# Performance work log

Hardware: AMD Instinct MI355X
Metric: run time of the kernel (lower is better)

The kernel has to match this reference:

```python
import jax, jax.numpy as jnp
import numpy as np

C = 16       # celltypes
N = 20000    # nodes per PPI graph
D = 192      # in_channels == out_channels*heads (residual constraint)
H = 3        # node_heads
CO = 64      # out_channels per head
E = 320000   # edges per PPI graph
T = 32       # tissue nodes
K = 8        # neighbors per tissue
M = C + T    # metagraph nodes
R = 4        # metagraph relations
EM = 256     # edges per metagraph relation
S = 128      # sem_att_channels
TU = 100     # tissue_update iterations


def setup_inputs():
    key = jax.random.key(0)
    k = jax.random.split(key, 16)
    g = lambda kk, shp, sc: jax.random.normal(kk, shp, jnp.float32) * sc
    return {
        "ppi_x": g(k[0], (C, N, D), 1.0),
        "metagraph_x": g(k[1], (M, D), 1.0),
        "ppi_lin": g(k[2], (C, D, H * CO), 0.07),
        "ppi_att_src": g(k[3], (C, H, CO), 0.1),
        "ppi_att_dst": g(k[4], (C, H, CO), 0.1),
        "ppi_bias": jnp.zeros((C, H * CO), jnp.float32),
        "meta_lin": g(k[5], (R, H * CO, H * CO), 0.07),
        "meta_att_src": g(k[6], (R, H, CO), 0.1),
        "meta_att_dst": g(k[7], (R, H, CO), 0.1),
        "meta_bias": jnp.zeros((R, H * CO), jnp.float32),
        "W_sem": g(k[8], (H * CO, S), 0.08),
        "b_sem": jnp.zeros((S,), jnp.float32),
        "q_sem": g(k[9], (S,), 0.1),
        "ppi_edges": jax.random.randint(k[10], (C, 2, E), 0, N, dtype=jnp.int32),
        "meta_edges": jax.random.randint(k[11], (R, 2, EM), 0, M, dtype=jnp.int32),
        "tissue_nb": jax.random.randint(k[12], (T, K), 0, M, dtype=jnp.int32),
    }


def gat(x, lin, att_s, att_d, bias, edge, n):
    """PyG-style GATConv, concat heads. x:[n,Din], edge:[2,E] (src,dst)."""
    h = (x @ lin).reshape(n, H, CO)
    a_s = (h * att_s).sum(-1)   # [n,H]
    a_d = (h * att_d).sum(-1)
    src, dst = edge[0], edge[1]
    e = jax.nn.leaky_relu(a_s[src] + a_d[dst], negative_slope=0.2)  # [E,H]
    emax = jax.lax.stop_gradient(jax.ops.segment_max(e, dst, num_segments=n))
    emax = jnp.where(jnp.isfinite(emax), emax, 0.0)
    ex = jnp.exp(e - emax[dst])
    denom = jax.ops.segment_sum(ex, dst, num_segments=n)          # [n,H]
    out = jax.ops.segment_sum(ex[:, :, None] * h[src], dst, num_segments=n)
    out = out / jnp.where(denom > 0.0, denom, 1.0)[:, :, None]
    return out.reshape(n, H * CO) + bias


def sem_attention(out, W, b, q):
    """Semantic attention over relations. out:[M,R,Dh]."""
    w = jnp.tanh(jnp.einsum('mrd,ds->mrs', out, W) + b)
    beta = jax.nn.softmax(jnp.einsum('mrs,s->mr', w, q), axis=1)
    return jnp.einsum('mrd,mr->md', out, beta)


def forward(ppi_x, metagraph_x, ppi_lin, ppi_att_src, ppi_att_dst, ppi_bias,
            meta_lin, meta_att_src, meta_att_dst, meta_bias,
            W_sem, b_sem, q_sem, ppi_edges, meta_edges, tissue_nb):
    mx = metagraph_x
    # residual GAT per celltype, mean-pooled into the metagraph celltype row
    for c in range(C):
        att = ppi_x[c] + gat(ppi_x[c], ppi_lin[c], ppi_att_src[c], ppi_att_dst[c],
                             ppi_bias[c], ppi_edges[c], N)
        mx = mx.at[c].add(att.mean(0))
    # sequential (Gauss-Seidel) tissue-neighbor mean diffusion, TU sweeps
    def step(m, t):
        return m.at[C + t].set(m[tissue_nb[t]].mean(0)), None
    def sweep(m, _):
        m, _ = jax.lax.scan(step, m, jnp.arange(T))
        return m, None
    mx, _ = jax.lax.scan(sweep, mx, None, length=TU)
    # multi-relation metagraph GAT + semantic attention fusion
    outs = jnp.stack([gat(mx, meta_lin[r], meta_att_src[r], meta_att_dst[r],
                          meta_bias[r], meta_edges[r], M) for r in range(R)], axis=1)
    outs = jax.nn.relu(outs)  # torch applies relu after stacking
    return sem_attention(outs, W_sem, b_sem, q_sem)


def reference(ppi_x, metagraph_x, ppi_lin, ppi_att_src, ppi_att_dst, ppi_bias,
              meta_lin, meta_att_src, meta_att_dst, meta_bias,
              W_sem, b_sem, q_sem, ppi_edges, meta_edges, tissue_nb):
    return forward(ppi_x, metagraph_x, ppi_lin, ppi_att_src, ppi_att_dst, ppi_bias,
                   meta_lin, meta_att_src, meta_att_dst, meta_bias,
                   W_sem, b_sem, q_sem, ppi_edges, meta_edges, tissue_nb)
```

## Files before the change

kernel.cpp:

```cpp
#include <hip/hip_runtime.h>

#define CT 16
#define NN 20000
#define EE 320000
#define MM 48
#define RR 4
#define EMM 256
#define NRANGE 64
#define NPR 313
#define CAP 5632
#define MAGIC 13721941ULL

#define OFF_MEANX 0
#define OFF_P     3072
#define OFF_CNTD  12288
#define OFF_CNTS  13312
#define ZERO_FLOATS 14336
#define OFF_COMB  14336
#define OFF_AS    2574336
#define OFF_AD    3854336
#define OFF_U     5134336
#define OFF_V     5143552
#define OFF_MX    5152768
#define OFF_HH    5161984
#define OFF_OUTS  5198848
#define OFF_BIND  5235712
#define OFF_BINS  11002880
#define OFF_W     16770048
#define OFF_MX2   16772352

__device__ inline unsigned bucket_of(int d) {
    return (unsigned)(((unsigned long long)(unsigned)d * MAGIC) >> 32);
}

__global__ __launch_bounds__(192) void k_prep(const float* __restrict__ lin,
        const float* __restrict__ as_g, const float* __restrict__ ad_g,
        float* __restrict__ U, float* __restrict__ V, float* __restrict__ zws) {
    int c = blockIdx.x, d = threadIdx.x;
    int gt = c * 192 + d;
    for (int o = gt; o < ZERO_FLOATS; o += 16 * 192) zws[o] = 0.f;
    const float* L  = lin + ((size_t)c * 192 + d) * 192;
    const float* As = as_g + c * 192;
    const float* Ad = ad_g + c * 192;
#pragma unroll
    for (int h = 0; h < 3; ++h) {
        float u = 0.f, v = 0.f;
        for (int j = 0; j < 64; ++j) {
            float lv = L[h * 64 + j];
            u += lv * As[h * 64 + j];
            v += lv * Ad[h * 64 + j];
        }
        U[c * 576 + h * 192 + d] = u;
        V[c * 576 + h * 192 + d] = v;
    }
}

__global__ __launch_bounds__(256) void k_front(const int* __restrict__ edges,
        int* __restrict__ cntD, int* __restrict__ cntS,
        int* __restrict__ binD, int* __restrict__ binS,
        const float* __restrict__ x, const float* __restrict__ U,
        const float* __restrict__ V, float* __restrict__ a_s,
        float* __restrict__ a_d, float* __restrict__ meanx) {
    __shared__ __align__(16) float smem[3456];
    int tid = threadIdx.x;
    if (blockIdx.x < 1024) {
        int wg = blockIdx.x;
        int ct = (wg & 7) * 2 + ((wg >> 3) & 1);
        int part = wg >> 4;
        int wave = tid >> 6;
        int* histD = (int*)smem;
        int* histS = histD + 256;
        int* curD  = histS + 256;
        int* curS  = curD + 64;
        if (tid < NRANGE) {
            histD[0 * 64 + tid] = 0; histD[1 * 64 + tid] = 0;
            histD[2 * 64 + tid] = 0; histD[3 * 64 + tid] = 0;
            histS[0 * 64 + tid] = 0; histS[1 * 64 + tid] = 0;
            histS[2 * 64 + tid] = 0; histS[3 * 64 + tid] = 0;
        }
        __syncthreads();
        const int* srcp = edges + (size_t)ct * 2 * EE;
        const int* dstp = srcp + EE;
        const int4* s4 = (const int4*)srcp;
        const int4* d4 = (const int4*)dstp;
        int base4 = part * 1250;
        for (int i = tid; i < 1250; i += 256) {
            int4 dv = d4[base4 + i];
            int4 sv = s4[base4 + i];
            atomicAdd(&histD[wave * 64 + bucket_of(dv.x)], 1);
            atomicAdd(&histD[wave * 64 + bucket_of(dv.y)], 1);
            atomicAdd(&histD[wave * 64 + bucket_of(dv.z)], 1);
            atomicAdd(&histD[wave * 64 + bucket_of(dv.w)], 1);
            atomicAdd(&histS[wave * 64 + bucket_of(sv.x)], 1);
            atomicAdd(&histS[wave * 64 + bucket_of(sv.y)], 1);
            atomicAdd(&histS[wave * 64 + bucket_of(sv.z)], 1);
            atomicAdd(&histS[wave * 64 + bucket_of(sv.w)], 1);
        }
        __syncthreads();
        if (tid < NRANGE) {
            int t = histD[tid] + histD[64 + tid] + histD[128 + tid] + histD[192 + tid];
            curD[tid] = atomicAdd(&cntD[ct * NRANGE + tid], t);
            int t2 = histS[tid] + histS[64 + tid] + histS[128 + tid] + histS[192 + tid];
            curS[tid] = atomicAdd(&cntS[ct * NRANGE + tid], t2);
        }
        __syncthreads();
        int* bD = binD + (size_t)ct * NRANGE * CAP;
        int* bS = binS + (size_t)ct * NRANGE * CAP;
#define EMIT2(ss, dd) { int pk = ((ss) << 15) | (dd); \
        unsigned bd = bucket_of(dd); int so = atomicAdd(&curD[bd], 1); \
        if (so < CAP) bD[bd * CAP + so] = pk; \
        unsigned bs = bucket_of(ss); int s2 = atomicAdd(&curS[bs], 1); \
        if (s2 < CAP) bS[bs * CAP + s2] = pk; }
        for (int i = tid; i < 1250; i += 256) {
            int4 dv = d4[base4 + i];
            int4 sv = s4[base4 + i];
            EMIT2(sv.x, dv.x); EMIT2(sv.y, dv.y); EMIT2(sv.z, dv.z); EMIT2(sv.w, dv.w);
        }
#undef EMIT2
    } else {
        int idx = blockIdx.x - 1024;
        int c = idx & 15;
        int start = (idx >> 4) * 160;
        int lane = tid & 63;
        int wave = tid >> 6;
        float* A = smem;
        float* blk = smem + 3264;
        if (tid < 192) blk[tid] = 0.f;
        float u0[3], u1[3], u2[3], v0[3], v1[3], v2[3];
#pragma unroll
        for (int h = 0; h < 3; ++h) {
            u0[h] = U[c * 576 + h * 192 + lane];
            u1[h] = U[c * 576 + h * 192 + 64 + lane];
            u2[h] = U[c * 576 + h * 192 + 128 + lane];
            v0[h] = V[c * 576 + h * 192 + lane];
            v1[h] = V[c * 576 + h * 192 + 64 + lane];
            v2[h] = V[c * 576 + h * 192 + 128 + lane];
        }
        __syncthreads();
        const float* xc = x + (size_t)c * NN * 192;
        float* asn = a_s + (size_t)c * NN * 4;
        float* adn = a_d + (size_t)c * NN * 4;
        float m0 = 0.f, m1 = 0.f, m2 = 0.f;
        float* Aa = A + (wave * 2) * 408;
        float* Ab = A + (wave * 2 + 1) * 408;
        int rrow = lane >> 3, seg = lane & 7;
        for (int i = 0; i < 20; ++i) {
            int na = start + wave + 8 * i;
            int nb = na + 4;
            const float* xa = xc + (size_t)na * 192;
            const float* xb = xc + (size_t)nb * 192;
            float xa0 = xa[lane], xa1 = xa[64 + lane], xa2 = xa[128 + lane];
            float xb0 = xb[lane], xb1 = xb[64 + lane], xb2 = xb[128 + lane];
            m0 += xa0 + xb0; m1 += xa1 + xb1; m2 += xa2 + xb2;
            Aa[0 * 68 + lane] = xa0 * u0[0] + xa1 * u1[0] + xa2 * u2[0];
            Aa[1 * 68 + lane] = xa0 * u0[1] + xa1 * u1[1] + xa2 * u2[1];
            Aa[2 * 68 + lane] = xa0 * u0[2] + xa1 * u1[2] + xa2 * u2[2];
            Aa[3 * 68 + lane] = xa0 * v0[0] + xa1 * v1[0] + xa2 * v2[0];
            Aa[4 * 68 + lane] = xa0 * v0[1] + xa1 * v1[1] + xa2 * v2[1];
            Aa[5 * 68 + lane] = xa0 * v0[2] + xa1 * v1[2] + xa2 * v2[2];
            Ab[0 * 68 + lane] = xb0 * u0[0] + xb1 * u1[0] + xb2 * u2[0];
            Ab[1 * 68 + lane] = xb0 * u0[1] + xb1 * u1[1] + xb2 * u2[1];
            Ab[2 * 68 + lane] = xb0 * u0[2] + xb1 * u1[2] + xb2 * u2[2];
            Ab[3 * 68 + lane] = xb0 * v0[0] + xb1 * v1[0] + xb2 * v2[0];
            Ab[4 * 68 + lane] = xb0 * v0[1] + xb1 * v1[1] + xb2 * v2[1];
            Ab[5 * 68 + lane] = xb0 * v0[2] + xb1 * v1[2] + xb2 * v2[2];
            float sa = 0.f, sb = 0.f;
            if (lane < 48) {
                const float4* pa = (const float4*)(Aa + rrow * 68 + seg * 8);
                const float4* pb = (const float4*)(Ab + rrow * 68 + seg * 8);
                float4 a0 = pa[0], a1 = pa[1];
                float4 b0 = pb[0], b1 = pb[1];
                sa = ((a0.x + a0.y) + (a0.z + a0.w)) + ((a1.x + a1.y) + (a1.z + a1.w));
                sb = ((b0.x + b0.y) + (b0.z + b0.w)) + ((b1.x + b1.y) + (b1.z + b1.w));
            }
            sa += __shfl_xor(sa, 1, 64); sb += __shfl_xor(sb, 1, 64);
            sa += __shfl_xor(sa, 2, 64); sb += __shfl_xor(sb, 2, 64);
            sa += __shfl_xor(sa, 4, 64); sb += __shfl_xor(sb, 4, 64);
            if (lane < 48 && seg == 0) {
                if (rrow < 3) { asn[na * 4 + rrow] = sa;     asn[nb * 4 + rrow] = sb; }
                else          { adn[na * 4 + rrow - 3] = sa; adn[nb * 4 + rrow - 3] = sb; }
            }
        }
        atomicAdd(&blk[lane], m0);
        atomicAdd(&blk[64 + lane], m1);
        atomicAdd(&blk[128 + lane], m2);
        __syncthreads();
        if (tid < 192) atomicAdd(&meanx[c * 192 + tid], blk[tid]);
    }
}

__device__ inline void map_ct(int wg, int& ct, int& j) {
    int xcd = wg & 7;
    ct = xcd * 2 + ((wg >> 3) & 1);
    j = wg >> 4;
}

__global__ __launch_bounds__(512) void k_eden_b(const int* __restrict__ bin,
        const int* __restrict__ cnt, const float* __restrict__ a_s,
        const float* __restrict__ a_d, float* __restrict__ comb) {
    int ct, bkt;
    map_ct(blockIdx.x, ct, bkt);
    int lo = bkt * NPR;
    int nnode = NN - lo < NPR ? NN - lo : NPR;
    int tid = threadIdx.x;
    __shared__ float adl[NPR * 3];
    __shared__ float den[NPR * 3];
    const float4* as4 = (const float4*)(a_s + (size_t)ct * NN * 4);
    const float4* ad4 = (const float4*)(a_d + (size_t)ct * NN * 4);
    for (int m = tid; m < nnode; m += 512) {
        float4 v = ad4[lo + m];
        adl[m * 3] = v.x; adl[m * 3 + 1] = v.y; adl[m * 3 + 2] = v.z;
    }
    for (int o = tid; o < nnode * 3; o += 512) den[o] = 0.f;
    __syncthreads();
    int n = cnt[ct * NRANGE + bkt]; if (n > CAP) n = CAP;
    const int* bc = bin + ((size_t)ct * NRANGE + bkt) * CAP;
    for (int i = tid; i < n; i += 512) {
        int v = bc[i];
        int d = v & 32767, s = v >> 15;
        int dl = d - lo;
        float4 av = as4[s];
        float e0 = av.x + adl[dl * 3];     e0 = e0 >= 0.f ? e0 : 0.2f * e0;
        float e1 = av.y + adl[dl * 3 + 1]; e1 = e1 >= 0.f ? e1 : 0.2f * e1;
        float e2 = av.z + adl[dl * 3 + 2]; e2 = e2 >= 0.f ? e2 : 0.2f * e2;
        atomicAdd(&den[dl * 3],     __expf(e0));
        atomicAdd(&den[dl * 3 + 1], __expf(e1));
        atomicAdd(&den[dl * 3 + 2], __expf(e2));
    }
    __syncthreads();
    float4* cb = (float4*)(comb + (size_t)ct * NN * 8);
    for (int m = tid; m < nnode; m += 512) {
        float d0 = den[m * 3], d1 = den[m * 3 + 1], d2 = den[m * 3 + 2];
        float4 a, b;
        a.x = adl[m * 3]; a.y = adl[m * 3 + 1]; a.z = adl[m * 3 + 2]; a.w = 0.f;
        b.x = d0 > 0.f ? 1.f / d0 : 0.f;
        b.y = d1 > 0.f ? 1.f / d1 : 0.f;
        b.z = d2 > 0.f ? 1.f / d2 : 0.f;
        b.w = 0.f;
        cb[(size_t)(lo + m) * 2]     = a;
        cb[(size_t)(lo + m) * 2 + 1] = b;
    }
}

__global__ __launch_bounds__(512) void k_es_p(const int* __restrict__ bin,
        const int* __restrict__ cnt, const float* __restrict__ a_s,
        const float* __restrict__ comb, const float* __restrict__ x,
        float* __restrict__ p, const int* __restrict__ nb,
        float* __restrict__ Wout) {
    __shared__ __align__(16) float smem[6912];
    int tid = threadIdx.x;
    if (blockIdx.x == 1024) {
        float* B0 = smem;
        float* B1 = smem + 2304;
        float* B2 = smem + 4608;
        float* B[3] = {B0, B1, B2};
        for (int o = tid; o < 2304; o += 512) {
            float idv = ((o / 48) == (o % 48)) ? 1.f : 0.f;
            B0[o] = idv;
            B1[o] = idv;
        }
        __syncthreads();
        if (tid < 48) {
            int j = tid;
            for (int t = 0; t < 32; ++t) {
                float acc = 0.f;
#pragma unroll
                for (int k = 0; k < 8; ++k) {
                    int idx = nb[t * 8 + k];
                    acc += B0[idx * 48 + j];
                }
                B0[(16 + t) * 48 + j] = acc * 0.125f;
            }
        }
        __syncthreads();
        int iP = 0, iR = 1, iT = 2;
        int e = 100;
        while (e) {
            if (e & 1) {
                for (int o = tid; o < 2304; o += 512) {
                    int rr = o / 48, cc = o - rr * 48;
                    float acc = 0.f;
                    for (int k = 0; k < 48; ++k) acc += B[iR][rr * 48 + k] * B[iP][k * 48 + cc];
                    B[iT][o] = acc;
                }
                __syncthreads();
                int t_ = iR; iR = iT; iT = t_;
            }
            e >>= 1;
            if (e) {
                for (int o = tid; o < 2304; o += 512) {
                    int rr = o / 48, cc = o - rr * 48;
                    float acc = 0.f;
                    for (int k = 0; k < 48; ++k) acc += B[iP][rr * 48 + k] * B[iP][k * 48 + cc];
                    B[iT][o] = acc;
                }
                __syncthreads();
                int t_ = iP; iP = iT; iT = t_;
            }
        }
        for (int o = tid; o < 2304; o += 512) Wout[o] = B[iR][o];
        return;
    }
    int ct, bkt;
    map_ct(blockIdx.x, ct, bkt);
    int lo = bkt * NPR;
    int nnode = NN - lo < NPR ? NN - lo : NPR;
    float* asl = smem;
    float* sl  = smem + 960;
    float* blk = smem + 1920;
    const float4* as4 = (const float4*)(a_s + (size_t)ct * NN * 4);
    const float4* cb  = (const float4*)(comb + (size_t)ct * NN * 8);
    for (int m = tid; m < nnode; m += 512) {
        float4 v = as4[lo + m];
        asl[m * 3] = v.x; asl[m * 3 + 1] = v.y; asl[m * 3 + 2] = v.z;
    }
    for (int o = tid; o < nnode * 3; o += 512) sl[o] = 0.f;
    for (int o = tid; o < 576; o += 512) blk[o] = 0.f;
    __syncthreads();
    int n = cnt[ct * NRANGE + bkt]; if (n > CAP) n = CAP;
    const int* bc = bin + ((size_t)ct * NRANGE + bkt) * CAP;
    for (int i = tid; i < n; i += 512) {
        int v = bc[i];
        int d = v & 32767, s = v >> 15;
        int slc = s - lo;
        float4 av = cb[(size_t)d * 2];
        float4 dv = cb[(size_t)d * 2 + 1];
        float e0 = asl[slc * 3]     + av.x; e0 = e0 >= 0.f ? e0 : 0.2f * e0;
        float e1 = asl[slc * 3 + 1] + av.y; e1 = e1 >= 0.f ? e1 : 0.2f * e1;
        float e2 = asl[slc * 3 + 2] + av.z; e2 = e2 >= 0.f ? e2 : 0.2f * e2;
        atomicAdd(&sl[slc * 3],     __expf(e0) * dv.x);
        atomicAdd(&sl[slc * 3 + 1], __expf(e1) * dv.y);
        atomicAdd(&sl[slc * 3 + 2], __expf(e2) * dv.z);
    }
    __syncthreads();
    int lane = tid & 63;
    int wave = tid >> 6;
    const float* xc = x + (size_t)ct * NN * 192;
    float a00 = 0, a01 = 0, a02 = 0, a10 = 0, a11 = 0, a12 = 0, a20 = 0, a21 = 0, a22 = 0;
    for (int m = wave; m < nnode; m += 8) {
        float s0 = sl[m * 3], s1 = sl[m * 3 + 1], s2 = sl[m * 3 + 2];
        const float* xr = xc + (size_t)(lo + m) * 192;
        float x0 = xr[lane], x1 = xr[64 + lane], x2 = xr[128 + lane];
        a00 += s0 * x0; a01 += s0 * x1; a02 += s0 * x2;
        a10 += s1 * x0; a11 += s1 * x1; a12 += s1 * x2;
        a20 += s2 * x0; a21 += s2 * x1; a22 += s2 * x2;
    }
    atomicAdd(&blk[0 * 192 + lane], a00);
    atomicAdd(&blk[0 * 192 + 64 + lane], a01);
    atomicAdd(&blk[0 * 192 + 128 + lane], a02);
    atomicAdd(&blk[1 * 192 + lane], a10);
    atomicAdd(&blk[1 * 192 + 64 + lane], a11);
    atomicAdd(&blk[1 * 192 + 128 + lane], a12);
    atomicAdd(&blk[2 * 192 + lane], a20);
    atomicAdd(&blk[2 * 192 + 64 + lane], a21);
    atomicAdd(&blk[2 * 192 + 128 + lane], a22);
    __syncthreads();
    for (int o = tid; o < 576; o += 512) atomicAdd(&p[ct * 576 + o], blk[o]);
}

__global__ __launch_bounds__(192) void k_mx(const float* __restrict__ mgx,
        const float* __restrict__ meanx, const float* __restrict__ p,
        const float* __restrict__ lin, const float* __restrict__ bias,
        float* __restrict__ mx) {
    int m = blockIdx.x, j = threadIdx.x;
    if (m < CT) {
        int h = j >> 6;
        const float* ph = p + m * 576 + h * 192;
        const float* L = lin + (size_t)m * 36864;
        float acc = 0.f;
        for (int k = 0; k < 192; ++k) acc += ph[k] * L[k * 192 + j];
        mx[m * 192 + j] = mgx[m * 192 + j] + (meanx[m * 192 + j] + acc) * (1.f / NN)
                          + bias[m * 192 + j];
    } else {
        mx[m * 192 + j] = mgx[m * 192 + j];
    }
}

__global__ __launch_bounds__(192) void k_tapply(const float* __restrict__ W,
        const float* __restrict__ mx, float* __restrict__ mx2) {
    int m = blockIdx.x, j = threadIdx.x;
    if (m < CT) {
        mx2[m * 192 + j] = mx[m * 192 + j];
    } else {
        float acc = 0.f;
        for (int k = 0; k < 48; ++k) acc += W[m * 48 + k] * mx[k * 192 + j];
        mx2[m * 192 + j] = acc;
    }
}

__global__ __launch_bounds__(192) void k_meta_h(const float* __restrict__ mx,
        const float* __restrict__ lin, float* __restrict__ hh) {
    int r = blockIdx.x, m = blockIdx.y, j = threadIdx.x;
    const float* L = lin + (size_t)r * 36864;
    const float* xr = mx + m * 192;
    float acc = 0.f;
    for (int k = 0; k < 192; ++k) acc += xr[k] * L[k * 192 + j];
    hh[((size_t)r * 48 + m) * 192 + j] = acc;
}

__global__ __launch_bounds__(256) void k_meta_edge(const float* __restrict__ hh,
        const float* __restrict__ att_s, const float* __restrict__ att_d,
        const float* __restrict__ bias, const int* __restrict__ edges,
        float* __restrict__ outs) {
    int r = blockIdx.x;
    int tid = threadIdx.x;
    __shared__ float as_[48][3], ad_[48][3], den[48][3];
    const float* hr = hh + (size_t)r * 48 * 192;
    float* og = outs + (size_t)r * 48 * 192;
    if (tid < 144) {
        int m = tid / 3, h = tid % 3;
        const float* As = att_s + r * 192 + h * 64;
        const float* Ad = att_d + r * 192 + h * 64;
        float s_ = 0.f, d_ = 0.f;
        for (int j = 0; j < 64; ++j) {
            float hv = hr[m * 192 + h * 64 + j];
            s_ += hv * As[j]; d_ += hv * Ad[j];
        }
        as_[m][h] = s_; ad_[m][h] = d_;
        den[m][h] = 0.f;
    }
    for (int o = tid; o < 9216; o += 256) og[o] = bias[r * 192 + (o % 192)];
    __syncthreads();
    int s = edges[(size_t)r * 2 * EMM + tid];
    int d = edges[(size_t)r * 2 * EMM + EMM + tid];
    float e0 = as_[s][0] + ad_[d][0]; e0 = e0 >= 0.f ? e0 : 0.2f * e0;
    float e1 = as_[s][1] + ad_[d][1]; e1 = e1 >= 0.f ? e1 : 0.2f * e1;
    float e2 = as_[s][2] + ad_[d][2]; e2 = e2 >= 0.f ? e2 : 0.2f * e2;
    float ex0 = __expf(e0), ex1 = __expf(e1), ex2 = __expf(e2);
    atomicAdd(&den[d][0], ex0);
    atomicAdd(&den[d][1], ex1);
    atomicAdd(&den[d][2], ex2);
    __syncthreads();
    float w0 = ex0 / den[d][0], w1 = ex1 / den[d][1], w2 = ex2 / den[d][2];
    const float* hs = hr + s * 192;
    float* od = og + d * 192;
    for (int j = 0; j < 64; ++j)        atomicAdd(&od[j], w0 * hs[j]);
    for (int j = 64; j < 128; ++j)      atomicAdd(&od[j], w1 * hs[j]);
    for (int j = 128; j < 192; ++j)     atomicAdd(&od[j], w2 * hs[j]);
}

__global__ __launch_bounds__(128) void k_sem(const float* __restrict__ outs,
        const float* __restrict__ W, const float* __restrict__ b,
        const float* __restrict__ q, float* __restrict__ out) {
    int m = blockIdx.x, s = threadIdx.x;
    __shared__ float ro[4][192];
    __shared__ float red[4][128];
    __shared__ float beta[4];
    for (int o = s; o < 768; o += 128) {
        int r = o / 192, d = o - r * 192;
        float v = outs[((size_t)r * 48 + m) * 192 + d];
        ro[r][d] = v > 0.f ? v : 0.f;
    }
    __syncthreads();
    float p0 = 0, p1 = 0, p2 = 0, p3 = 0;
    for (int d = 0; d < 192; ++d) {
        float wv = W[d * 128 + s];
        p0 += ro[0][d] * wv; p1 += ro[1][d] * wv; p2 += ro[2][d] * wv; p3 += ro[3][d] * wv;
    }
    float bb = b[s], qq = q[s];
    red[0][s] = tanhf(p0 + bb) * qq;
    red[1][s] = tanhf(p1 + bb) * qq;
    red[2][s] = tanhf(p2 + bb) * qq;
    red[3][s] = tanhf(p3 + bb) * qq;
    __syncthreads();
    for (int off = 64; off >= 1; off >>= 1) {
        if (s < off) {
            red[0][s] += red[0][s + off];
            red[1][s] += red[1][s + off];
            red[2][s] += red[2][s + off];
            red[3][s] += red[3][s + off];
        }
        __syncthreads();
    }
    if (s == 0) {
        float s0 = red[0][0], s1 = red[1][0], s2 = red[2][0], s3 = red[3][0];
        float mx4 = fmaxf(fmaxf(s0, s1), fmaxf(s2, s3));
        float e0 = __expf(s0 - mx4), e1 = __expf(s1 - mx4);
        float e2 = __expf(s2 - mx4), e3 = __expf(s3 - mx4);
        float inv = 1.f / (e0 + e1 + e2 + e3);
        beta[0] = e0 * inv; beta[1] = e1 * inv; beta[2] = e2 * inv; beta[3] = e3 * inv;
    }
    __syncthreads();
    for (int d = s; d < 192; d += 128) {
        float acc = ro[0][d] * beta[0] + ro[1][d] * beta[1]
                  + ro[2][d] * beta[2] + ro[3][d] * beta[3];
        out[m * 192 + d] = acc;
    }
}

extern "C" void kernel_launch(void* const* d_in, const int* in_sizes, int n_in,
                              void* d_out, int out_size, void* d_ws, size_t ws_size,
                              hipStream_t stream) {
    const float* ppi_x    = (const float*)d_in[0];
    const float* mgx      = (const float*)d_in[1];
    const float* ppi_lin  = (const float*)d_in[2];
    const float* ppi_as   = (const float*)d_in[3];
    const float* ppi_ad   = (const float*)d_in[4];
    const float* ppi_b    = (const float*)d_in[5];
    const float* meta_lin = (const float*)d_in[6];
    const float* meta_as  = (const float*)d_in[7];
    const float* meta_ad  = (const float*)d_in[8];
    const float* meta_b   = (const float*)d_in[9];
    const float* W_sem    = (const float*)d_in[10];
    const float* b_sem    = (const float*)d_in[11];
    const float* q_sem    = (const float*)d_in[12];
    const int*   ppi_e    = (const int*)d_in[13];
    const int*   meta_e   = (const int*)d_in[14];
    const int*   tnb      = (const int*)d_in[15];

    float* ws   = (float*)d_ws;
    float* mnx  = ws + OFF_MEANX;
    float* pac  = ws + OFF_P;
    int*   cntD = (int*)(ws + OFF_CNTD);
    int*   cntS = (int*)(ws + OFF_CNTS);
    float* comb = ws + OFF_COMB;
    float* a_s  = ws + OFF_AS;
    float* a_d  = ws + OFF_AD;
    float* U    = ws + OFF_U;
    float* V    = ws + OFF_V;
    float* mx   = ws + OFF_MX;
    float* hh   = ws + OFF_HH;
    float* outs = ws + OFF_OUTS;
    int*   binD = (int*)(ws + OFF_BIND);
    int*   binS = (int*)(ws + OFF_BINS);
    float* Wt   = ws + OFF_W;
    float* mx2  = ws + OFF_MX2;

    k_prep<<<16, 192, 0, stream>>>(ppi_lin, ppi_as, ppi_ad, U, V, ws);
    k_front<<<3024, 256, 0, stream>>>(ppi_e, cntD, cntS, binD, binS,
                                      ppi_x, U, V, a_s, a_d, mnx);
    k_eden_b<<<1024, 512, 0, stream>>>(binD, cntD, a_s, a_d, comb);
    k_es_p<<<1025, 512, 0, stream>>>(binS, cntS, a_s, comb, ppi_x, pac, tnb, Wt);
    k_mx<<<48, 192, 0, stream>>>(mgx, mnx, pac, ppi_lin, ppi_b, mx);
    k_tapply<<<48, 192, 0, stream>>>(Wt, mx, mx2);
    k_meta_h<<<dim3(4, 48), 192, 0, stream>>>(mx2, meta_lin, hh);
    k_meta_edge<<<4, 256, 0, stream>>>(hh, meta_as, meta_ad, meta_b, meta_e, outs);
    k_sem<<<48, 128, 0, stream>>>(outs, W_sem, b_sem, q_sem, (float*)d_out);
}
```

Measured before the change: 528.6 us.

## Move tissue-diffusion matrix power into k_front and exploit identity block structure

The single block that computes the 100-sweep diffusion operator by repeated squaring moves from k_es_p into the first block of k_front. It now stores only the 32 tissue rows and uses the identity structure of the first 16 columns, which cuts the matmul work and the shared memory it needs. k_es_p drops its oversized shared buffer and switches to right-sized static arrays, which may allow more occupancy. The serial block may still sit on the critical path inside k_front, and only the tissue rows of Wout are written, so the celltype rows must already hold valid values.

```diff
diff --git a/kernel.cpp b/kernel.cpp
--- a/kernel.cpp
+++ b/kernel.cpp
@@ -60,11 +60,73 @@
         int* __restrict__ binD, int* __restrict__ binS,
         const float* __restrict__ x, const float* __restrict__ U,
         const float* __restrict__ V, float* __restrict__ a_s,
-        float* __restrict__ a_d, float* __restrict__ meanx) {
+        float* __restrict__ a_d, float* __restrict__ meanx,
+        const int* __restrict__ nb, float* __restrict__ Wout) {
     __shared__ __align__(16) float smem[3456];
     int tid = threadIdx.x;
-    if (blockIdx.x < 1024) {
-        int wg = blockIdx.x;
+    if (blockIdx.x == 0) {
+        float* P  = smem;
+        float* Rm = smem + 1536;
+        for (int o = tid; o < 1536; o += 256) {
+            int i = o / 48, j = o - i * 48;
+            float idv = (j == 16 + i) ? 1.f : 0.f;
+            P[o] = idv;
+            Rm[o] = idv;
+        }
+        __syncthreads();
+        if (tid < 48) {
+            int j = tid;
+            for (int t = 0; t < 32; ++t) {
+                float acc = 0.f;
+#pragma unroll
+                for (int k = 0; k < 8; ++k) {
+                    int idx = nb[t * 8 + k];
+                    acc += (idx < 16) ? (j == idx ? 1.f : 0.f)
+                                      : P[(idx - 16) * 48 + j];
+                }
+                P[t * 48 + j] = acc * 0.125f;
+            }
+        }
+        __syncthreads();
+        int e = 100;
+        float r[6];
+        while (e) {
+            if (e & 1) {
+#pragma unroll
+                for (int q = 0; q < 6; ++q) {
+                    int o = tid + q * 256;
+                    int i = o / 48, j = o - i * 48;
+                    float acc = (j < 16) ? Rm[i * 48 + j] : 0.f;
+                    for (int t = 0; t < 32; ++t) acc += Rm[i * 48 + 16 + t] * P[t * 48 + j];
+                    r[q] = acc;
+                }
+                __syncthreads();
+#pragma unroll
+                for (int q = 0; q < 6; ++q) Rm[tid + q * 256] = r[q];
+                __syncthreads();
+            }
+            e >>= 1;
+            if (e) {
+#pragma unroll
+                for (int q = 0; q < 6; ++q) {
+                    int o = tid + q * 256;
+                    int i = o / 48, j = o - i * 48;
+                    float acc = (j < 16) ? P[i * 48 + j] : 0.f;
+                    for (int t = 0; t < 32; ++t) acc += P[i * 48 + 16 + t] * P[t * 48 + j];
+                    r[q] = acc;
+                }
+                __syncthreads();
+#pragma unroll
+                for (int q = 0; q < 6; ++q) P[tid + q * 256] = r[q];
+                __syncthreads();
+            }
+        }
+        for (int o = tid; o < 1536; o += 256) {
+            int i = o / 48, j = o - i * 48;
+            Wout[(16 + i) * 48 + j] = Rm[o];
+        }
+    } else if (blockIdx.x < 1025) {
+        int wg = blockIdx.x - 1;
         int ct = (wg & 7) * 2 + ((wg >> 3) & 1);
         int part = wg >> 4;
         int wave = tid >> 6;
@@ -118,7 +180,7 @@
         }
 #undef EMIT2
     } else {
-        int idx = blockIdx.x - 1024;
+        int idx = blockIdx.x - 1025;
         int c = idx & 15;
         int start = (idx >> 4) * 160;
         int lane = tid & 63;
@@ -146,9 +208,9 @@
         int rrow = lane >> 3, seg = lane & 7;
         for (int i = 0; i < 20; ++i) {
             int na = start + wave + 8 * i;
-            int nb = na + 4;
+            int nb_ = na + 4;
             const float* xa = xc + (size_t)na * 192;
-            const float* xb = xc + (size_t)nb * 192;
+            const float* xb = xc + (size_t)nb_ * 192;
             float xa0 = xa[lane], xa1 = xa[64 + lane], xa2 = xa[128 + lane];
             float xb0 = xb[lane], xb1 = xb[64 + lane], xb2 = xb[128 + lane];
             m0 += xa0 + xb0; m1 += xa1 + xb1; m2 += xa2 + xb2;
@@ -177,8 +239,8 @@
             sa += __shfl_xor(sa, 2, 64); sb += __shfl_xor(sb, 2, 64);
             sa += __shfl_xor(sa, 4, 64); sb += __shfl_xor(sb, 4, 64);
             if (lane < 48 && seg == 0) {
-                if (rrow < 3) { asn[na * 4 + rrow] = sa;     asn[nb * 4 + rrow] = sb; }
-                else          { adn[na * 4 + rrow - 3] = sa; adn[nb * 4 + rrow - 3] = sb; }
+                if (rrow < 3) { asn[na * 4 + rrow] = sa;      asn[nb_ * 4 + rrow] = sb; }
+                else          { adn[na * 4 + rrow - 3] = sa;  adn[nb_ * 4 + rrow - 3] = sb; }
             }
         }
         atomicAdd(&blk[lane], m0);
@@ -245,69 +307,15 @@
 __global__ __launch_bounds__(512) void k_es_p(const int* __restrict__ bin,
         const int* __restrict__ cnt, const float* __restrict__ a_s,
         const float* __restrict__ comb, const float* __restrict__ x,
-        float* __restrict__ p, const int* __restrict__ nb,
-        float* __restrict__ Wout) {
-    __shared__ __align__(16) float smem[6912];
-    int tid = threadIdx.x;
-    if (blockIdx.x == 1024) {
-        float* B0 = smem;
-        float* B1 = smem + 2304;
-        float* B2 = smem + 4608;
-        float* B[3] = {B0, B1, B2};
-        for (int o = tid; o < 2304; o += 512) {
-            float idv = ((o / 48) == (o % 48)) ? 1.f : 0.f;
-            B0[o] = idv;
-            B1[o] = idv;
-        }
-        __syncthreads();
-        if (tid < 48) {
-            int j = tid;
-            for (int t = 0; t < 32; ++t) {
-                float acc = 0.f;
-#pragma unroll
-                for (int k = 0; k < 8; ++k) {
-                    int idx = nb[t * 8 + k];
-                    acc += B0[idx * 48 + j];
-                }
-                B0[(16 + t) * 48 + j] = acc * 0.125f;
-            }
-        }
-        __syncthreads();
-        int iP = 0, iR = 1, iT = 2;
-        int e = 100;
-        while (e) {
-            if (e & 1) {
-                for (int o = tid; o < 2304; o += 512) {
-                    int rr = o / 48, cc = o - rr * 48;
-                    float acc = 0.f;
-                    for (int k = 0; k < 48; ++k) acc += B[iR][rr * 48 + k] * B[iP][k * 48 + cc];
-                    B[iT][o] = acc;
-                }
-                __syncthreads();
-                int t_ = iR; iR = iT; iT = t_;
-            }
-            e >>= 1;
-            if (e) {
-                for (int o = tid; o < 2304; o += 512) {
-                    int rr = o / 48, cc = o - rr * 48;
-                    float acc = 0.f;
-                    for (int k = 0; k < 48; ++k) acc += B[iP][rr * 48 + k] * B[iP][k * 48 + cc];
-                    B[iT][o] = acc;
-                }
-                __syncthreads();
-                int t_ = iP; iP = iT; iT = t_;
-            }
-        }
-        for (int o = tid; o < 2304; o += 512) Wout[o] = B[iR][o];
-        return;
-    }
+        float* __restrict__ p) {
     int ct, bkt;
     map_ct(blockIdx.x, ct, bkt);
     int lo = bkt * NPR;
     int nnode = NN - lo < NPR ? NN - lo : NPR;
-    float* asl = smem;
-    float* sl  = smem + 960;
-    float* blk = smem + 1920;
+    int tid = threadIdx.x;
+    __shared__ float asl[NPR * 3];
+    __shared__ float sl[NPR * 3];
+    __shared__ float blk[576];
     const float4* as4 = (const float4*)(a_s + (size_t)ct * NN * 4);
     const float4* cb  = (const float4*)(comb + (size_t)ct * NN * 8);
     for (int m = tid; m < nnode; m += 512) {
@@ -527,10 +535,10 @@
     float* mx2  = ws + OFF_MX2;
 
     k_prep<<<16, 192, 0, stream>>>(ppi_lin, ppi_as, ppi_ad, U, V, ws);
-    k_front<<<3024, 256, 0, stream>>>(ppi_e, cntD, cntS, binD, binS,
-                                      ppi_x, U, V, a_s, a_d, mnx);
+    k_front<<<3025, 256, 0, stream>>>(ppi_e, cntD, cntS, binD, binS,
+                                      ppi_x, U, V, a_s, a_d, mnx, tnb, Wt);
     k_eden_b<<<1024, 512, 0, stream>>>(binD, cntD, a_s, a_d, comb);
-    k_es_p<<<1025, 512, 0, stream>>>(binS, cntS, a_s, comb, ppi_x, pac, tnb, Wt);
+    k_es_p<<<1024, 512, 0, stream>>>(binS, cntS, a_s, comb, ppi_x, pac);
     k_mx<<<48, 192, 0, stream>>>(mgx, mnx, pac, ppi_lin, ppi_b, mx);
     k_tapply<<<48, 192, 0, stream>>>(Wt, mx, mx2);
     k_meta_h<<<dim3(4, 48), 192, 0, stream>>>(mx2, meta_lin, hh);
```

Result: slower. 593.9 us (+12.4%).
